# Kernel optimization log

Measured on AMD Instinct MI355X. Metric: run time of the kernel, lower is better.

Reference implementation:

```python
import jax, jax.numpy as jnp
import numpy as np
import math

B = 128        # batch (= bipartite matching N)
L = 16         # detector layers (MAX_LAYER)
E = 768        # n_embd
D = E // 2     # RFF target_dim
H = 12         # n_head
HD = E // H    # head_size
NL = 6         # n_layer
SEQ = 12       # tokens after concats: 3+3 -> 6 -> +currentLayer -> 12
MAX_LAYER = L
LN_EPS = 1e-3  # keras LayerNormalization default


def setup_inputs() -> dict:
    key = jax.random.key(0)
    ks = jax.random.split(key, 8)
    inp = {}
    inp["X"] = jax.random.normal(ks[0], (B, L, 3), dtype=jnp.float32) * 50.0
    inp["targets"] = jax.random.normal(ks[1], (B, L, 3), dtype=jnp.float32)
    # RandomFourierFeatures params (random per-call in original; fixed here):
    # x: xmin=-160,xmax=160,n=9*1024 ; y: n=12*512 ; dE: xmin=0,xmax=230,n=2300
    specs = [(-160.0, 160.0, 9 * 1024), (-160.0, 160.0, 12 * 512), (0.0, 230.0, 2300)]
    om, ph = [], []
    for i, (xmin, xmax, n) in enumerate(specs):
        k1, k2 = jax.random.split(jax.random.fold_in(ks[2], i))
        omin = 2.0 * math.pi / (xmax - xmin)
        lo, hi = math.log(omin / n), math.log(omin)
        om.append(jnp.exp(jax.random.uniform(k1, (D,), minval=lo, maxval=hi)))
        ph.append(jax.random.uniform(k2, (D,)))  # B ~ U(0,1)*scale, scale=1
    inp["omegas"] = jnp.stack(om).astype(jnp.float32)  # (3, D)
    inp["phases"] = jnp.stack(ph).astype(jnp.float32)  # (3, D)
    # np.random.permutation per layer-step, fixed here
    inp["perms"] = jnp.stack(
        [jax.random.permutation(jax.random.fold_in(ks[3], i), B) for i in range(L - 1)]
    ).astype(jnp.int32)  # (L-1, B)
    # transformer weights (stacked over layers)
    kk = jax.random.split(ks[4], 16)
    s = 0.02
    inp["Wq"] = jax.random.normal(kk[0], (NL, E, H, HD)) * s
    inp["bq"] = jnp.zeros((NL, H, HD))
    inp["Wk"] = jax.random.normal(kk[1], (NL, E, H, HD)) * s
    inp["bk"] = jnp.zeros((NL, H, HD))
    inp["Wv"] = jax.random.normal(kk[2], (NL, E, H, HD)) * s
    inp["bv"] = jnp.zeros((NL, H, HD))
    inp["Wo"] = jax.random.normal(kk[3], (NL, H, HD, E)) * s
    inp["bo"] = jnp.zeros((NL, E))
    inp["ln1g"] = jnp.ones((NL, E)); inp["ln1b"] = jnp.zeros((NL, E))
    inp["ln2g"] = jnp.ones((NL, E)); inp["ln2b"] = jnp.zeros((NL, E))
    inp["W1"] = jax.random.normal(kk[4], (NL, E, 4 * E)) * s
    inp["b1f"] = jnp.zeros((NL, 4 * E))
    inp["W2"] = jax.random.normal(kk[5], (NL, 4 * E, E)) * s
    inp["b2f"] = jnp.zeros((NL, E))
    inp["lnfg"] = jnp.ones((E,)); inp["lnfb"] = jnp.zeros((E,))
    inp["Wout"] = jax.random.normal(kk[6], (SEQ * E, 3)) * s
    inp["bout"] = jnp.zeros((3,))
    return inp


def _ln(x, g, b):
    mu = jnp.mean(x, -1, keepdims=True)
    v = jnp.var(x, -1, keepdims=True)
    return (x - mu) * jax.lax.rsqrt(v + LN_EPS) * g + b


def _greedy_match(cost):
    """Greedy bipartite matching: sort all NxN costs ascending, assign first-come.
    Returns row_to_col_match_vec (N,) int32."""
    N = cost.shape[0]
    order = jnp.argsort(cost.reshape(-1))

    def step(carry, k):
        row, col = carry
        i = k // N
        j = k % N
        ok = (row[i] == -1) & (col[j] == -1)
        row = row.at[i].set(jnp.where(ok, j, row[i]))
        col = col.at[j].set(jnp.where(ok, i, col[j]))
        return (row, col), None

    init = (jnp.full((N,), -1, jnp.int32), jnp.full((N,), -1, jnp.int32))
    (row, _), _ = jax.lax.scan(step, init, order)
    return row


def _forward(X, targets, omegas, phases, perms, Wq, bq, Wk, bk, Wv, bv, Wo, bo,
             ln1g, ln1b, ln2g, ln2b, W1, b1f, W2, b2f, lnfg, lnfb, Wout, bout):
    # RFF: (B,L,3) -> (B,L,3,D)
    XS = jnp.cos(X[..., None] * omegas[None, None, :, :] + phases[None, None, :, :])
    losses = []
    scale = 1.0 / math.sqrt(HD)
    for lidx in range(1, L):
        xc = XS[:, -lidx]        # (B,3,D)
        xp = XS[:, -lidx - 1]    # (B,3,D)
        x = jnp.concatenate([xc, xp], axis=2)            # (B,3,E)
        y = targets[:, -lidx + 1]                        # (B,3)
        y_prev = jnp.broadcast_to(y[:, :, None], (B, 3, E))
        x = jnp.concatenate([x, y_prev], axis=1)         # (B,6,E)
        cur = jnp.full_like(x, float(MAX_LAYER - lidx))
        x = jnp.concatenate([x, cur], axis=1)            # (B,12,E)
        x = x[perms[lidx - 1]]                           # batch permutation
        for l in range(NL):
            h = _ln(x, ln1g[l], ln1b[l])
            q = jnp.einsum('bse,ehd->bshd', h, Wq[l]) + bq[l]
            k = jnp.einsum('bse,ehd->bshd', h, Wk[l]) + bk[l]
            v = jnp.einsum('bse,ehd->bshd', h, Wv[l]) + bv[l]
            att = jax.nn.softmax(jnp.einsum('bqhd,bkhd->bhqk', q, k) * scale, axis=-1)
            o = jnp.einsum('bhqk,bkhd->bqhd', att, v)
            x = x + (jnp.einsum('bqhd,hde->bqe', o, Wo[l]) + bo[l])
            h = _ln(x, ln2g[l], ln2b[l])
            x = x + (jnp.maximum(h @ W1[l] + b1f[l], 0.0) @ W2[l] + b2f[l])
        x = _ln(x, lnfg, lnfb).reshape(B, SEQ * E)
        logits = x @ Wout + bout                         # (B,3)
        tgt = targets[:, -lidx]                          # (B,3)
        cost = jnp.sqrt(jnp.sum((logits[:, None, :] - tgt[None, :, :]) ** 2, axis=-1) + 1e-12)
        m = _greedy_match(jax.lax.stop_gradient(cost))
        lm = logits[m]                                   # gather per original
        losses.append(jnp.mean((lm - tgt) ** 2))
    return jnp.mean(jnp.stack(losses))


def reference(X, targets, omegas, phases, perms, Wq, bq, Wk, bk, Wv, bv, Wo, bo,
              ln1g, ln1b, ln2g, ln2b, W1, b1f, W2, b2f, lnfg, lnfb, Wout, bout):
    return _forward(X, targets, omegas, phases, perms, Wq, bq, Wk, bk, Wv, bv, Wo, bo,
                    ln1g, ln1b, ln2g, ln2b, W1, b1f, W2, b2f, lnfg, lnfb, Wout, bout)
```

## Files before the change

### kernel.cpp

```cpp
#include <hip/hip_runtime.h>
#include <hip/hip_bf16.h>
#include <math.h>

#define B_   128
#define L_   16
#define E_   768
#define D_   384
#define H_   12
#define HD_  64
#define NL_  6
#define SEQ_ 12
#define LN_EPS 0.001f
#define WLS   7077888
#define BQS   2304

typedef __attribute__((ext_vector_type(8))) short bf16x8;
typedef __attribute__((ext_vector_type(4))) float f32x4;
typedef unsigned long long u64;

#define GLOAD_LDS16(g, l) \
    __builtin_amdgcn_global_load_lds((__attribute__((address_space(1))) const void*)(g), \
                                     (__attribute__((address_space(3))) void*)(l), 16, 0, 0)

__global__ __launch_bounds__(256) void k_x0(const float* __restrict__ X,
                                            const float* __restrict__ targets,
                                            const int* __restrict__ perms,
                                            const float* __restrict__ om,
                                            const float* __restrict__ ph,
                                            float* __restrict__ x, int cb, int ntok) {
    int i = blockIdx.x * 256 + threadIdx.x;
    if (i >= ntok*E_) return;
    int e   = i % E_;
    int tok = i / E_;
    int s   = tok % SEQ_;
    int bi  = (tok / SEQ_) % B_;
    int c   = tok / (SEQ_*B_);
    int cl  = cb + c;
    int lidx = cl + 1;
    int pb  = perms[cl*B_ + bi];
    float val;
    if (s < 3) {
        int t  = (e < D_) ? (L_ - lidx) : (L_ - lidx - 1);
        int dd = (e < D_) ? e : (e - D_);
        float xv = X[(pb*L_ + t)*3 + s];
        val = cosf(xv * om[s*D_ + dd] + ph[s*D_ + dd]);
    } else if (s < 6) {
        int t = (17 - lidx) & 15;
        val = targets[(pb*L_ + t)*3 + (s - 3)];
    } else {
        val = (float)(L_ - lidx);
    }
    x[i] = val;
}

__global__ __launch_bounds__(256) void k_ln(const float* __restrict__ x,
                                            const float* __restrict__ g,
                                            const float* __restrict__ b,
                                            __hip_bfloat16* __restrict__ h) {
    int gi = blockIdx.x * 256 + threadIdx.x;
    int tok = gi >> 6, lane = gi & 63;
    const float4* xr = (const float4*)(x + (size_t)tok * E_);
    float4 v0 = xr[lane], v1 = xr[lane + 64], v2 = xr[lane + 128];
    float s = v0.x+v0.y+v0.z+v0.w + v1.x+v1.y+v1.z+v1.w + v2.x+v2.y+v2.z+v2.w;
    #pragma unroll
    for (int o = 32; o > 0; o >>= 1) s += __shfl_xor(s, o, 64);
    float mu = s * (1.0f / E_);
    v0.x-=mu; v0.y-=mu; v0.z-=mu; v0.w-=mu;
    v1.x-=mu; v1.y-=mu; v1.z-=mu; v1.w-=mu;
    v2.x-=mu; v2.y-=mu; v2.z-=mu; v2.w-=mu;
    float q = v0.x*v0.x+v0.y*v0.y+v0.z*v0.z+v0.w*v0.w
            + v1.x*v1.x+v1.y*v1.y+v1.z*v1.z+v1.w*v1.w
            + v2.x*v2.x+v2.y*v2.y+v2.z*v2.z+v2.w*v2.w;
    #pragma unroll
    for (int o = 32; o > 0; o >>= 1) q += __shfl_xor(q, o, 64);
    float rstd = rsqrtf(q * (1.0f / E_) + LN_EPS);
    const float4* g4 = (const float4*)g;
    const float4* b4 = (const float4*)b;
    ushort4* h4 = (ushort4*)(h + (size_t)tok * E_);
    #pragma unroll
    for (int k = 0; k < 3; k++) {
        float4 v = (k == 0) ? v0 : (k == 1) ? v1 : v2;
        float4 gg = g4[lane + k*64], bb = b4[lane + k*64];
        ushort4 o;
        o.x = __bfloat16_as_ushort(__float2bfloat16(v.x * rstd * gg.x + bb.x));
        o.y = __bfloat16_as_ushort(__float2bfloat16(v.y * rstd * gg.y + bb.y));
        o.z = __bfloat16_as_ushort(__float2bfloat16(v.z * rstd * gg.z + bb.z));
        o.w = __bfloat16_as_ushort(__float2bfloat16(v.w * rstd * gg.w + bb.w));
        h4[lane + k*64] = o;
    }
}

__global__ __launch_bounds__(256) void k_cvt(const float* __restrict__ Wq,
                                             const float* __restrict__ Wk,
                                             const float* __restrict__ Wv,
                                             const float* __restrict__ Wo,
                                             const float* __restrict__ W1,
                                             const float* __restrict__ W2,
                                             const float* __restrict__ bq,
                                             const float* __restrict__ bk,
                                             const float* __restrict__ bv,
                                             __hip_bfloat16* __restrict__ wl0,
                                             float* __restrict__ bqkv0, int lbase) {
    int bid = blockIdx.x;
    int l   = lbase + bid / 6913;
    bid %= 6913;
    __hip_bfloat16* wl = wl0 + (size_t)(l - lbase) * WLS;
    float* bqkv = bqkv0 + (l - lbase) * BQS;
    int tid = threadIdx.x;
    if (bid == 6912) {
        for (int i = tid; i < 2304; i += 256) {
            float v = (i < 768) ? bq[l*768 + i] : (i < 1536) ? bk[l*768 + i - 768]
                                                             : bv[l*768 + i - 1536];
            bqkv[i] = v;
        }
        return;
    }
    const float* src; __hip_bfloat16* dst; int K, N, ti, tj;
    if (bid < 1728) {
        int part = bid / 576, idx = bid % 576;
        const float* srcs[3] = {Wq, Wk, Wv};
        src = srcs[part] + (size_t)l*768*768; dst = wl + (size_t)part*768*768;
        K = 768; N = 768; tj = idx % 24; ti = idx / 24;
    } else if (bid < 2304) {
        int idx = bid - 1728;
        src = Wo + (size_t)l*768*768; dst = wl + 1769472;
        K = 768; N = 768; tj = idx % 24; ti = idx / 24;
    } else if (bid < 4608) {
        int idx = bid - 2304;
        src = W1 + (size_t)l*768*3072; dst = wl + 2359296;
        K = 768; N = 3072; tj = idx % 96; ti = idx / 96;
    } else {
        int idx = bid - 4608;
        src = W2 + (size_t)l*3072*768; dst = wl + 4718592;
        K = 3072; N = 768; tj = idx % 24; ti = idx / 24;
    }
    __shared__ float tbuf[32][33];
    int tx = tid & 31, ty = tid >> 5;
    #pragma unroll
    for (int p = 0; p < 4; p++) {
        int k = ti*32 + ty + p*8, n = tj*32 + tx;
        tbuf[ty + p*8][tx] = src[(size_t)k*N + n];
    }
    __syncthreads();
    #pragma unroll
    for (int p = 0; p < 4; p++) {
        int n = tj*32 + ty + p*8, k = ti*32 + tx;
        dst[(size_t)n*K + k] = __float2bfloat16(tbuf[tx][ty + p*8]);
    }
}

#define MFMA_BF16(a, b, c) __builtin_amdgcn_mfma_f32_16x16x32_bf16(a, b, c, 0, 0, 0)

__global__ __launch_bounds__(512) void k_gemm256(const __hip_bfloat16* __restrict__ A,
                                                 const __hip_bfloat16* __restrict__ Bt,
                                                 const float* __restrict__ bias,
                                                 void* __restrict__ Cp,
                                                 int K, int ldb, int ldc, int flags) {
    __shared__ __align__(16) char smem[131072];
    const int tid  = threadIdx.x;
    const int lane = tid & 63;
    const int wid  = tid >> 6;
    const int wr   = wid >> 2;
    const int wc   = wid & 3;
    const int m0   = blockIdx.y * 256;
    const int n0   = blockIdx.x * 256;
    const int fr   = lane & 15, fkg = lane >> 4, sx = fr & 7;
    const int NT   = K >> 6;

    const int srow = tid >> 3;
    const int skc  = 8 * ((tid & 7) ^ (srow & 7));

    f32x4 acc[8][4] = {};

    auto stage = [&](int kt, int buf) {
        char* base = smem + buf*65536;
        const int kk = kt*64 + skc;
        GLOAD_LDS16(A  + (size_t)(m0 +       srow) * K   + kk, base +         tid*16);
        GLOAD_LDS16(A  + (size_t)(m0 +  64 + srow) * K   + kk, base +  8192 + tid*16);
        GLOAD_LDS16(A  + (size_t)(m0 + 128 + srow) * K   + kk, base + 16384 + tid*16);
        GLOAD_LDS16(A  + (size_t)(m0 + 192 + srow) * K   + kk, base + 24576 + tid*16);
        GLOAD_LDS16(Bt + (size_t)(n0 +       srow) * ldb + kk, base + 32768 + tid*16);
        GLOAD_LDS16(Bt + (size_t)(n0 +  64 + srow) * ldb + kk, base + 40960 + tid*16);
        GLOAD_LDS16(Bt + (size_t)(n0 + 128 + srow) * ldb + kk, base + 49152 + tid*16);
        GLOAD_LDS16(Bt + (size_t)(n0 + 192 + srow) * ldb + kk, base + 57344 + tid*16);
    };
    auto ldA = [&](int buf, int i, int ks) -> bf16x8 {
        int row = wr*128 + i*16 + fr;
        return *(const bf16x8*)(smem + buf*65536 + row*128 + (((ks*4 + fkg) ^ sx) << 4));
    };
    auto ldB = [&](int buf, int j, int ks) -> bf16x8 {
        int row = wc*64 + j*16 + fr;
        return *(const bf16x8*)(smem + buf*65536 + 32768 + row*128 + (((ks*4 + fkg) ^ sx) << 4));
    };

    stage(0, 0);
    __syncthreads();

    for (int kt = 0; kt < NT; ++kt) {
        const int cur = kt & 1;
        if (kt + 1 < NT) stage(kt + 1, cur ^ 1);
        bf16x8 b[4][2];
        #pragma unroll
        for (int j = 0; j < 4; j++) { b[j][0] = ldB(cur, j, 0); b[j][1] = ldB(cur, j, 1); }
        #pragma unroll
        for (int ih = 0; ih < 2; ih++) {
            bf16x8 a[4][2];
            #pragma unroll
            for (int i = 0; i < 4; i++) {
                a[i][0] = ldA(cur, ih*4 + i, 0);
                a[i][1] = ldA(cur, ih*4 + i, 1);
            }
            __builtin_amdgcn_s_setprio(1);
            #pragma unroll
            for (int i = 0; i < 4; i++)
                #pragma unroll
                for (int j = 0; j < 4; j++) {
                    acc[ih*4+i][j] = MFMA_BF16(a[i][0], b[j][0], acc[ih*4+i][j]);
                    acc[ih*4+i][j] = MFMA_BF16(a[i][1], b[j][1], acc[ih*4+i][j]);
                }
            __builtin_amdgcn_s_setprio(0);
        }
        __syncthreads();
    }

    const int colL = lane & 15, rowg = (lane >> 4) * 4;
    #pragma unroll
    for (int i = 0; i < 8; i++) {
        #pragma unroll
        for (int j = 0; j < 4; j++) {
            int col = n0 + wc*64 + j*16 + colL;
            float bv = bias ? bias[col] : 0.0f;
            #pragma unroll
            for (int r = 0; r < 4; r++) {
                int row = m0 + wr*128 + i*16 + rowg + r;
                float v = acc[i][j][r] + bv;
                if (flags & 4) v = fmaxf(v, 0.0f);
                size_t off = (size_t)row * ldc + col;
                if (flags & 1)      ((__hip_bfloat16*)Cp)[off] = __float2bfloat16(v);
                else if (flags & 2) ((float*)Cp)[off] += v;
                else                ((float*)Cp)[off] = v;
            }
        }
    }
}

__global__ __launch_bounds__(256) void k_attn(const __hip_bfloat16* __restrict__ qkv,
                                              __hip_bfloat16* __restrict__ o) {
    __shared__ float qs[SEQ_][HD_], ks[SEQ_][HD_], vs[SEQ_][HD_];
    __shared__ float att[SEQ_][SEQ_];
    int blk = blockIdx.x;
    int hh  = blk % H_;
    int cbb = blk / H_;
    int t = threadIdx.x;
    if (t < 96) {
        int s = t >> 3, c = (t & 7) * 8;
        size_t base = (size_t)(cbb*SEQ_ + s) * 2304 + hh*64 + c;
        bf16x8 q8 = *(const bf16x8*)(qkv + base);
        bf16x8 k8 = *(const bf16x8*)(qkv + base + 768);
        bf16x8 v8 = *(const bf16x8*)(qkv + base + 1536);
        #pragma unroll
        for (int j = 0; j < 8; j++) {
            qs[s][c+j] = __uint_as_float((unsigned)(unsigned short)q8[j] << 16);
            ks[s][c+j] = __uint_as_float((unsigned)(unsigned short)k8[j] << 16);
            vs[s][c+j] = __uint_as_float((unsigned)(unsigned short)v8[j] << 16);
        }
    }
    __syncthreads();
    if (t < SEQ_*SEQ_) {
        int qi = t / SEQ_, kj = t % SEQ_;
        float s = 0.f;
        #pragma unroll
        for (int d = 0; d < HD_; d++) s += qs[qi][d] * ks[kj][d];
        att[qi][kj] = s * 0.125f;
    }
    __syncthreads();
    if (t < SEQ_) {
        float mx = -1e30f;
        #pragma unroll
        for (int j = 0; j < SEQ_; j++) mx = fmaxf(mx, att[t][j]);
        float e[SEQ_]; float sum = 0.f;
        #pragma unroll
        for (int j = 0; j < SEQ_; j++) { e[j] = expf(att[t][j] - mx); sum += e[j]; }
        float inv = 1.f / sum;
        #pragma unroll
        for (int j = 0; j < SEQ_; j++) att[t][j] = e[j] * inv;
    }
    __syncthreads();
    for (int i = t; i < SEQ_*HD_; i += 256) {
        int s = i / HD_, d = i % HD_;
        float acc = 0.f;
        #pragma unroll
        for (int j = 0; j < SEQ_; j++) acc += att[s][j] * vs[j][d];
        o[(size_t)(cbb*SEQ_ + s) * 768 + hh*64 + d] = __float2bfloat16(acc);
    }
}

__global__ __launch_bounds__(256) void k_logits(const __hip_bfloat16* __restrict__ hfin,
                                                const float* __restrict__ Wout,
                                                const float* __restrict__ bout,
                                                float* __restrict__ logits, int cb) {
    __shared__ float red[3][256];
    int blk = blockIdx.x;
    int t = threadIdx.x;
    const __hip_bfloat16* row = hfin + (size_t)blk * SEQ_ * E_;
    float a0 = 0.f, a1 = 0.f, a2 = 0.f;
    for (int e = t; e < SEQ_*E_; e += 256) {
        float x = __bfloat162float(row[e]);
        a0 += x * Wout[e*3 + 0]; a1 += x * Wout[e*3 + 1]; a2 += x * Wout[e*3 + 2];
    }
    red[0][t] = a0; red[1][t] = a1; red[2][t] = a2;
    __syncthreads();
    for (int o = 128; o > 0; o >>= 1) {
        if (t < o) { red[0][t] += red[0][t+o]; red[1][t] += red[1][t+o]; red[2][t] += red[2][t+o]; }
        __syncthreads();
    }
    if (t < 3) logits[((size_t)cb*B_ + blk)*3 + t] = red[t][0] + bout[t];
}

__global__ __launch_bounds__(64) void k_match(const float* __restrict__ logits,
                                              const float* __restrict__ targets,
                                              float* __restrict__ losses) {
    __shared__ float cst[128 * 129];
    __shared__ float tg[128][3];
    __shared__ int mrow[128];
    int cl = blockIdx.x, lane = threadIdx.x;
    int lidx = cl + 1;
    for (int j = lane; j < 128; j += 64) {
        const float* tp = &targets[((size_t)j*L_ + (L_ - lidx)) * 3];
        tg[j][0] = tp[0]; tg[j][1] = tp[1]; tg[j][2] = tp[2];
    }
    __syncthreads();
    u64 kc[2];
    #pragma unroll
    for (int hh = 0; hh < 2; hh++) {
        int r = lane + hh*64;
        const float* lg = &logits[(cl*B_ + r) * 3];
        float l0 = lg[0], l1 = lg[1], l2 = lg[2];
        u64 best = ~0ull;
        for (int c = 0; c < 128; c++) {
            float d0 = l0 - tg[c][0], d1 = l1 - tg[c][1], d2 = l2 - tg[c][2];
            float cc = sqrtf(d0*d0 + d1*d1 + d2*d2 + 1e-12f);
            cst[r*129 + c] = cc;
            u64 key = ((u64)__float_as_uint(cc) << 14) | (unsigned)(r*128 + c);
            best = key < best ? key : best;
        }
        kc[hh] = best;
    }
    __syncthreads();
    u64 dead0 = 0, dead1 = 0;
    int done = 0;
    for (int trip = 0; trip < 16640 && done < 128; trip++) {
        u64 b = kc[0] < kc[1] ? kc[0] : kc[1];
        #pragma unroll
        for (int o = 32; o > 0; o >>= 1) {
            u64 x = __shfl_xor(b, o, 64);
            b = x < b ? x : b;
        }
        unsigned e  = (unsigned)b & 0x3fffu;
        unsigned wi = e >> 7, wj = e & 127;
        bool isDead = (((wj < 64) ? (dead0 >> wj) : (dead1 >> (wj - 64))) & 1ull) != 0;
        if (!isDead) {
            if ((wi & 63u) == (unsigned)lane) {
                mrow[wi] = (int)wj;
                kc[wi >> 6] = ~0ull;
            }
            if (wj < 64) dead0 |= 1ull << wj; else dead1 |= 1ull << (wj - 64);
            done++;
        } else {
            float c0 = cst[wi*129 + lane];
            float c1 = cst[wi*129 + lane + 64];
            bool d0b = ((dead0 >> lane) & 1ull) != 0;
            bool d1b = ((dead1 >> lane) & 1ull) != 0;
            u64 k0 = d0b ? ~0ull : (((u64)__float_as_uint(c0) << 14) | (unsigned)(wi*128 + lane));
            u64 k1 = d1b ? ~0ull : (((u64)__float_as_uint(c1) << 14) | (unsigned)(wi*128 + lane + 64));
            u64 nb = k0 < k1 ? k0 : k1;
            #pragma unroll
            for (int o = 32; o > 0; o >>= 1) {
                u64 x = __shfl_xor(nb, o, 64);
                nb = x < nb ? x : nb;
            }
            if ((wi & 63u) == (unsigned)lane) kc[wi >> 6] = nb;
        }
    }
    __syncthreads();
    float a = 0.f;
    #pragma unroll
    for (int hh = 0; hh < 2; hh++) {
        int r = lane + hh*64;
        const float* lg = &logits[(cl*B_ + mrow[r]) * 3];
        float d0 = lg[0]-tg[r][0], d1 = lg[1]-tg[r][1], d2 = lg[2]-tg[r][2];
        a += d0*d0 + d1*d1 + d2*d2;
    }
    #pragma unroll
    for (int o = 32; o > 0; o >>= 1) a += __shfl_xor(a, o, 64);
    if (lane == 0) losses[cl] = a * (1.0f / (B_*3));
}

__global__ void k_final(const float* __restrict__ losses, float* __restrict__ out) {
    float s = 0.f;
    for (int i = 0; i < 15; i++) s += losses[i];
    out[0] = s * (1.0f / 15.0f);
}

extern "C" void kernel_launch(void* const* d_in, const int* in_sizes, int n_in,
                              void* d_out, int out_size, void* d_ws, size_t ws_size,
                              hipStream_t stream) {
    (void)in_sizes; (void)n_in; (void)out_size;
    const float* X       = (const float*)d_in[0];
    const float* targets = (const float*)d_in[1];
    const float* omegas  = (const float*)d_in[2];
    const float* phases  = (const float*)d_in[3];
    const int*   perms   = (const int*)d_in[4];
    const float* Wq  = (const float*)d_in[5];
    const float* bq  = (const float*)d_in[6];
    const float* Wk  = (const float*)d_in[7];
    const float* bk  = (const float*)d_in[8];
    const float* Wv  = (const float*)d_in[9];
    const float* bv  = (const float*)d_in[10];
    const float* Wo  = (const float*)d_in[11];
    const float* bo  = (const float*)d_in[12];
    const float* ln1g = (const float*)d_in[13];
    const float* ln1b = (const float*)d_in[14];
    const float* ln2g = (const float*)d_in[15];
    const float* ln2b = (const float*)d_in[16];
    const float* W1  = (const float*)d_in[17];
    const float* b1f = (const float*)d_in[18];
    const float* W2  = (const float*)d_in[19];
    const float* b2f = (const float*)d_in[20];
    const float* lnfg = (const float*)d_in[21];
    const float* lnfb = (const float*)d_in[22];
    const float* Wout = (const float*)d_in[23];
    const float* bout = (const float*)d_in[24];

    int CL; bool hoist;
    if (ws_size >= 263000000ull)      { CL = 15; hoist = false; }
    else if (ws_size >= 169000000ull) { CL = 5;  hoist = true;  }
    else                              { CL = 5;  hoist = false; }
    int M = CL * B_ * SEQ_;
    bool perLayerCvt = (CL == 15) || !hoist;

    char* wsb = (char*)d_ws;
    size_t off = 0;
    auto alloc = [&](size_t bytes) {
        char* p = wsb + off;
        off += (bytes + 255) & ~(size_t)255;
        return p;
    };
    float*          x      = (float*)alloc((size_t)M*E_*4);
    __hip_bfloat16* h      = (__hip_bfloat16*)alloc((size_t)M*E_*2);
    __hip_bfloat16* qkvh   = (__hip_bfloat16*)alloc((size_t)M*3072*2);
    __hip_bfloat16* wl     = (__hip_bfloat16*)alloc((hoist ? 6 : 1) * (size_t)WLS*2);
    float*          bqkv   = (float*)alloc((hoist ? 6 : 1) * (size_t)BQS*4);
    float*          logits = (float*)alloc(23040);
    float*          losses = (float*)alloc(64);

    if (hoist)
        k_cvt<<<6*6913, 256, 0, stream>>>(Wq, Wk, Wv, Wo, W1, W2, bq, bk, bv, wl, bqkv, 0);

    dim3 gQKV(2304/256, M/256);
    dim3 gF1 (3072/256, M/256);
    dim3 gN  (768/256,  M/256);
    dim3 gLN (M/4);

    for (int cb = 0; cb < 15; cb += CL) {
        k_x0<<<(M*E_)/256, 256, 0, stream>>>(X, targets, perms, omegas, phases, x, cb, M);
        for (int l = 0; l < NL_; l++) {
            __hip_bfloat16* wlp = hoist ? wl + (size_t)l*WLS : wl;
            float*          bqp = hoist ? bqkv + l*BQS : bqkv;
            if (perLayerCvt)
                k_cvt<<<6913, 256, 0, stream>>>(Wq, Wk, Wv, Wo, W1, W2, bq, bk, bv, wlp, bqp, l);
            k_ln<<<gLN, 256, 0, stream>>>(x, ln1g + l*E_, ln1b + l*E_, h);
            k_gemm256<<<gQKV, 512, 0, stream>>>(h, wlp, bqp, qkvh, 768, 768, 2304, 1);
            k_attn<<<CL*B_*H_, 256, 0, stream>>>(qkvh, h);
            k_gemm256<<<gN, 512, 0, stream>>>(h, wlp + 1769472, bo + l*E_, x,
                                              768, 768, 768, 2);
            k_ln<<<gLN, 256, 0, stream>>>(x, ln2g + l*E_, ln2b + l*E_, h);
            k_gemm256<<<gF1, 512, 0, stream>>>(h, wlp + 2359296, b1f + l*3072, qkvh,
                                               768, 768, 3072, 1|4);
            k_gemm256<<<gN, 512, 0, stream>>>(qkvh, wlp + 4718592, b2f + l*E_, x,
                                              3072, 3072, 768, 2);
        }
        k_ln<<<gLN, 256, 0, stream>>>(x, lnfg, lnfb, h);
        k_logits<<<CL*B_, 256, 0, stream>>>(h, Wout, bout, logits, cb);
    }
    k_match<<<15, 64, 0, stream>>>(logits, targets, losses);
    k_final<<<1, 1, 0, stream>>>(losses, (float*)d_out);
}
```

Baseline: 5.097 ms.

## Swizzle GEMM tiles across XCDs and track top-two candidates in greedy match

The GEMM kernel remaps flat workgroup IDs so that consecutive tiles land on the same XCD, which is meant to improve L2 reuse of the A and B panels. The greedy matching kernel now keeps each row's best and second-best column keys, so that when a column is claimed most affected rows can fall back to their second choice instead of lazily re-scanning the row. Rows that run out of candidates are rescanned eagerly with a two-value wave reduction. This cuts the number of serial matching iterations to exactly 128, at the cost of a more complex per-step update.

Result: no change. 5.178 ms (+1.6%).

```diff
diff --git a/kernel.cpp b/kernel.cpp
--- a/kernel.cpp
+++ b/kernel.cpp
@@ -162,8 +162,16 @@
     const int wid  = tid >> 6;
     const int wr   = wid >> 2;
     const int wc   = wid & 3;
-    const int m0   = blockIdx.y * 256;
-    const int n0   = blockIdx.x * 256;
+
+    const int gx   = gridDim.x;
+    const int nwg  = gx * gridDim.y;
+    const int flat = blockIdx.y * gx + blockIdx.x;
+    const int q8   = nwg >> 3, r8 = nwg & 7;
+    const int xcd  = flat & 7, off8 = flat >> 3;
+    const int swz  = (xcd < r8 ? xcd*(q8+1) : r8*(q8+1) + (xcd-r8)*q8) + off8;
+    const int m0   = (swz / gx) * 256;
+    const int n0   = (swz % gx) * 256;
+
     const int fr   = lane & 15, fkg = lane >> 4, sx = fr & 7;
     const int NT   = K >> 6;
 
@@ -330,27 +338,27 @@
         tg[j][0] = tp[0]; tg[j][1] = tp[1]; tg[j][2] = tp[2];
     }
     __syncthreads();
-    u64 kc[2];
+    u64 m1[2], m2[2];
     #pragma unroll
     for (int hh = 0; hh < 2; hh++) {
         int r = lane + hh*64;
         const float* lg = &logits[(cl*B_ + r) * 3];
         float l0 = lg[0], l1 = lg[1], l2 = lg[2];
-        u64 best = ~0ull;
+        u64 b1 = ~0ull, b2 = ~0ull;
         for (int c = 0; c < 128; c++) {
             float d0 = l0 - tg[c][0], d1 = l1 - tg[c][1], d2 = l2 - tg[c][2];
             float cc = sqrtf(d0*d0 + d1*d1 + d2*d2 + 1e-12f);
             cst[r*129 + c] = cc;
             u64 key = ((u64)__float_as_uint(cc) << 14) | (unsigned)(r*128 + c);
-            best = key < best ? key : best;
-        }
-        kc[hh] = best;
+            if (key < b1)      { b2 = b1; b1 = key; }
+            else if (key < b2) { b2 = key; }
+        }
+        m1[hh] = b1; m2[hh] = b2;
     }
     __syncthreads();
     u64 dead0 = 0, dead1 = 0;
-    int done = 0;
-    for (int trip = 0; trip < 16640 && done < 128; trip++) {
-        u64 b = kc[0] < kc[1] ? kc[0] : kc[1];
+    for (int match = 0; match < 128; match++) {
+        u64 b = m1[0] < m1[1] ? m1[0] : m1[1];
         #pragma unroll
         for (int o = 32; o > 0; o >>= 1) {
             u64 x = __shfl_xor(b, o, 64);
@@ -358,28 +366,48 @@
         }
         unsigned e  = (unsigned)b & 0x3fffu;
         unsigned wi = e >> 7, wj = e & 127;
-        bool isDead = (((wj < 64) ? (dead0 >> wj) : (dead1 >> (wj - 64))) & 1ull) != 0;
-        if (!isDead) {
-            if ((wi & 63u) == (unsigned)lane) {
-                mrow[wi] = (int)wj;
-                kc[wi >> 6] = ~0ull;
+        if ((wi & 63u) == (unsigned)lane) {
+            mrow[wi] = (int)wj;
+            m1[wi >> 6] = ~0ull; m2[wi >> 6] = ~0ull;
+        }
+        if (wj < 64) dead0 |= 1ull << wj; else dead1 |= 1ull << (wj - 64);
+        bool need0 = false, need1 = false;
+        #pragma unroll
+        for (int h = 0; h < 2; h++) {
+            if (m2[h] != ~0ull && ((unsigned)m2[h] & 127u) == wj) m2[h] = ~0ull;
+            if (m1[h] != ~0ull && ((unsigned)m1[h] & 127u) == wj) {
+                if (m2[h] != ~0ull) { m1[h] = m2[h]; m2[h] = ~0ull; }
+                else {
+                    m1[h] = ~0ull;
+                    if (h == 0) need0 = true; else need1 = true;
+                }
             }
-            if (wj < 64) dead0 |= 1ull << wj; else dead1 |= 1ull << (wj - 64);
-            done++;
-        } else {
-            float c0 = cst[wi*129 + lane];
-            float c1 = cst[wi*129 + lane + 64];
+        }
+        u64 nb0 = __ballot(need0);
+        u64 nb1 = __ballot(need1);
+        while (nb0 | nb1) {
+            int R;
+            if (nb0) { R = __builtin_ctzll(nb0);      nb0 &= nb0 - 1; }
+            else     { R = __builtin_ctzll(nb1) + 64; nb1 &= nb1 - 1; }
+            float c0 = cst[R*129 + lane];
+            float c1 = cst[R*129 + lane + 64];
             bool d0b = ((dead0 >> lane) & 1ull) != 0;
             bool d1b = ((dead1 >> lane) & 1ull) != 0;
-            u64 k0 = d0b ? ~0ull : (((u64)__float_as_uint(c0) << 14) | (unsigned)(wi*128 + lane));
-            u64 k1 = d1b ? ~0ull : (((u64)__float_as_uint(c1) << 14) | (unsigned)(wi*128 + lane + 64));
-            u64 nb = k0 < k1 ? k0 : k1;
+            u64 k0 = d0b ? ~0ull : (((u64)__float_as_uint(c0) << 14) | (unsigned)(R*128 + lane));
+            u64 k1 = d1b ? ~0ull : (((u64)__float_as_uint(c1) << 14) | (unsigned)(R*128 + lane + 64));
+            u64 p1 = k0 < k1 ? k0 : k1;
+            u64 p2 = k0 < k1 ? k1 : k0;
             #pragma unroll
             for (int o = 32; o > 0; o >>= 1) {
-                u64 x = __shfl_xor(nb, o, 64);
-                nb = x < nb ? x : nb;
+                u64 q1 = __shfl_xor(p1, o, 64);
+                u64 q2 = __shfl_xor(p2, o, 64);
+                u64 lo  = p1 < q1 ? p1 : q1;
+                u64 hiA = p1 < q1 ? q1 : p1;
+                u64 hiB = p2 < q2 ? p2 : q2;
+                p1 = lo;
+                p2 = hiA < hiB ? hiA : hiB;
             }
-            if ((wi & 63u) == (unsigned)lane) kc[wi >> 6] = nb;
+            if ((R & 63) == lane) { m1[R >> 6] = p1; m2[R >> 6] = p2; }
         }
     }
     __syncthreads();
```
